# Performance work log

Measured on AMD Instinct MI355X. Metric: run time of the kernel, lower is better.

## Reference

```python
import jax, jax.numpy as jnp
import numpy as np

N = 100000   # nodes
E = 1600000  # edges (avg degree 16)
D = 128      # feature / hidden dim
C = 64       # classes
L = 4        # number of GCNII layers
ALPHA = 0.1
LAMDA = 0.5


def setup_inputs() -> dict:
    key = jax.random.key(0)
    ks = jax.random.split(key, 8)
    stdv = 1.0 / np.sqrt(D)
    x = jax.random.normal(ks[0], (N, D), jnp.float32)
    edge_src = jax.random.randint(ks[1], (E,), 0, N)
    edge_dst = jax.random.randint(ks[2], (E,), 0, N)
    edge_weight = jax.random.uniform(ks[3], (E,), jnp.float32)
    w_in = jax.random.uniform(ks[4], (D, D), jnp.float32, -stdv, stdv)
    b_in = jnp.zeros((D,), jnp.float32)
    gcn_w = jax.random.uniform(ks[5], (L, D, D), jnp.float32, -stdv, stdv)
    w_out = jax.random.uniform(ks[6], (D, C), jnp.float32, -stdv, stdv)
    b_out = jnp.zeros((C,), jnp.float32)
    return {"x": x, "edge_src": edge_src, "edge_dst": edge_dst,
            "edge_weight": edge_weight, "w_in": w_in, "b_in": b_in,
            "gcn_w": gcn_w, "w_out": w_out, "b_out": b_out}


def _spmm(edge_src, edge_dst, edge_weight, h):
    # torch.sparse.mm(adj, h): out[i] = sum_j adj[i,j] * h[j]
    # row = dst, col = src in COO terms.
    return jax.ops.segment_sum(edge_weight[:, None] * h[edge_src],
                               edge_dst, num_segments=N)


def reference(x, edge_src, edge_dst, edge_weight, w_in, b_in, gcn_w, w_out, b_out):
    h0 = jax.nn.relu(x @ w_in + b_in)          # [N, D] initial residual
    h = h0
    for l in range(L):
        # GCNConvII called with l_arg = l+1 -> theta = log(lamda/(l_arg+1) + 1)
        theta = float(np.log(LAMDA / (l + 2) + 1.0))
        hi = _spmm(edge_src, edge_dst, edge_weight, h)      # sparse SpMM
        support = (1.0 - ALPHA) * hi + ALPHA * h0           # initial-residual mix
        out = theta * (support @ gcn_w[l]) + (1.0 - theta) * support
        out = out + h                                       # identity residual
        h = jax.nn.relu(out)
    logits = h @ w_out + b_out                              # [N, C]
    return jax.nn.log_softmax(logits, axis=1)
```

## Files before the change

### kernel.cpp

```cpp
#include <hip/hip_runtime.h>
#include <hip/hip_fp16.h>
#include <math.h>

#define N_NODES 100000
#define N_EDGES 1600000
#define DIM     128
#define NCLS    64
#define ALPHA   0.1f

#define SCAN_B  98
#define NB      391
#define NF      ((size_t)N_NODES * DIM)
#define STRIPES (N_NODES / 16)
#define CHUNK   4096

typedef __attribute__((ext_vector_type(8))) _Float16 f16x8;
typedef __attribute__((ext_vector_type(4))) float    f32x4;

__device__ __forceinline__ __half2 u2h2(unsigned int u) {
    union { unsigned int u; __half2 h; } x; x.u = u; return x.h;
}
__device__ __forceinline__ unsigned int h22u(__half2 h) {
    union { unsigned int u; __half2 h; } x; x.h = h; return x.u;
}


__global__ __launch_bounds__(256) void k_hist(const int* __restrict__ dst,
                                              int* __restrict__ bucket_cnt) {
    __shared__ int hist[NB];
    int t = threadIdx.x;
    for (int b = t; b < NB; b += 256) hist[b] = 0;
    __syncthreads();
    int base = blockIdx.x * CHUNK;
    int end = min(base + CHUNK, N_EDGES);
    for (int i = base + t; i < end; i += 256)
        atomicAdd(&hist[dst[i] >> 8], 1);
    __syncthreads();
    for (int b = t; b < NB; b += 256)
        if (hist[b]) atomicAdd(&bucket_cnt[b], hist[b]);
}

__global__ __launch_bounds__(512) void k_scanb(const int* __restrict__ bucket_cnt,
                                               int* __restrict__ bucket_base,
                                               int* __restrict__ bucket_cursor) {
    __shared__ int s[512];
    int t = threadIdx.x;
    int v = (t < NB) ? bucket_cnt[t] : 0;
    s[t] = v;
    __syncthreads();
    for (int off = 1; off < 512; off <<= 1) {
        int u = (t >= off) ? s[t - off] : 0;
        __syncthreads();
        s[t] += u;
        __syncthreads();
    }
    if (t < NB) {
        int base = s[t] - v;
        bucket_base[t] = base;
        bucket_cursor[t] = base;
    }
    if (t == 0) bucket_base[NB] = N_EDGES;
}

__global__ __launch_bounds__(256) void k_part(const int* __restrict__ src,
                                              const int* __restrict__ dst,
                                              const float* __restrict__ ew,
                                              int* __restrict__ bucket_cursor,
                                              int2* __restrict__ ebuf) {
    __shared__ int lhist[NB], gbase[NB];
    int t = threadIdx.x;
    for (int b = t; b < NB; b += 256) lhist[b] = 0;
    __syncthreads();
    int base = blockIdx.x * CHUNK;
    int end = min(base + CHUNK, N_EDGES);
    for (int i = base + t; i < end; i += 256)
        atomicAdd(&lhist[dst[i] >> 8], 1);
    __syncthreads();
    for (int b = t; b < NB; b += 256) {
        int c = lhist[b];
        gbase[b] = c ? atomicAdd(&bucket_cursor[b], c) : 0;
        lhist[b] = 0;
    }
    __syncthreads();
    for (int i = base + t; i < end; i += 256) {
        int d = dst[i];
        int b = d >> 8;
        int r = atomicAdd(&lhist[b], 1);
        ebuf[gbase[b] + r] = make_int2(src[i] | ((d & 255) << 17),
                                       __float_as_int((1.0f - ALPHA) * ew[i]));
    }
}

__global__ __launch_bounds__(256) void k_deg(const int2* __restrict__ ebuf,
                                             const int* __restrict__ bucket_base,
                                             int* __restrict__ deg) {
    __shared__ int cnt[256];
    int t = threadIdx.x, b = blockIdx.x;
    cnt[t] = 0;
    __syncthreads();
    int beg = bucket_base[b], end = bucket_base[b + 1];
    for (int i = beg + t; i < end; i += 256)
        atomicAdd(&cnt[ebuf[i].x >> 17], 1);
    __syncthreads();
    int node = b * 256 + t;
    if (node < N_NODES) deg[node] = cnt[t];
}

__global__ __launch_bounds__(1024) void k_scan1(const int* __restrict__ deg,
                                                int* __restrict__ row_ptr,
                                                int* __restrict__ blocksum) {
    __shared__ int s[1024];
    int t = threadIdx.x;
    int i = blockIdx.x * 1024 + t;
    int v = (i < N_NODES) ? deg[i] : 0;
    s[t] = v;
    __syncthreads();
    for (int off = 1; off < 1024; off <<= 1) {
        int u = (t >= off) ? s[t - off] : 0;
        __syncthreads();
        s[t] += u;
        __syncthreads();
    }
    if (i < N_NODES) row_ptr[i] = s[t] - v;
    if (t == 1023) blocksum[blockIdx.x] = s[1023];
}

__global__ __launch_bounds__(128) void k_scan2(int* __restrict__ blocksum) {
    __shared__ int s[128];
    int t = threadIdx.x;
    int v = (t < SCAN_B) ? blocksum[t] : 0;
    s[t] = v;
    __syncthreads();
    for (int off = 1; off < 128; off <<= 1) {
        int u = (t >= off) ? s[t - off] : 0;
        __syncthreads();
        s[t] += u;
        __syncthreads();
    }
    if (t < SCAN_B) blocksum[t] = s[t] - v;
}

__global__ __launch_bounds__(1024) void k_scan3(int* __restrict__ row_ptr,
                                                const int* __restrict__ blocksum) {
    int t = threadIdx.x;
    int i = blockIdx.x * 1024 + t;
    if (i < N_NODES) row_ptr[i] += blocksum[blockIdx.x];
    if (i == 0) row_ptr[N_NODES] = N_EDGES;
}

__global__ __launch_bounds__(256) void k_scatter2(const int2* __restrict__ ebuf,
                                                  const int* __restrict__ bucket_base,
                                                  const int* __restrict__ row_ptr,
                                                  int2* __restrict__ colw) {
    __shared__ int lcur[256];
    int t = threadIdx.x, b = blockIdx.x;
    int node = b * 256 + t;
    lcur[t] = (node < N_NODES) ? row_ptr[node] : 0;
    __syncthreads();
    int beg = bucket_base[b], end = bucket_base[b + 1];
    for (int i = beg + t; i < end; i += 256) {
        int2 e = ebuf[i];
        int pos = atomicAdd(&lcur[e.x >> 17], 1);
        unsigned int w2 = h22u(__float2half2_rn(__int_as_float(e.y)));
        colw[pos] = make_int2(e.x & 0x1FFFF, (int)w2);
    }
}

__global__ void k_prepw(const float* __restrict__ gcnw, const float* __restrict__ wout,
                        const float* __restrict__ win, unsigned short* __restrict__ wp) {
    int tid = blockIdx.x * 256 + threadIdx.x;
    if (tid < 65536) {
        int l = tid >> 14;
        int r = tid & 16383;
        int j = r & 7, lane = (r >> 3) & 63, ch = (r >> 9) & 3, nt = r >> 11;
        int n = nt * 16 + (lane & 15);
        int k = ch * 32 + (lane >> 4) * 8 + j;
        wp[tid] = __half_as_ushort(__float2half(gcnw[l * 16384 + k * 128 + n]));
    } else if (tid < 73728) {
        int r = tid - 65536;
        int j = r & 7, lane = (r >> 3) & 63, ch = (r >> 9) & 3, nt = r >> 11;
        int n = nt * 16 + (lane & 15);
        int k = ch * 32 + (lane >> 4) * 8 + j;
        wp[tid] = __half_as_ushort(__float2half(wout[k * 64 + n]));
    } else if (tid < 90112) {
        int r = tid - 73728;
        int j = r & 7, lane = (r >> 3) & 63, ch = (r >> 9) & 3, nt = r >> 11;
        int n = nt * 16 + (lane & 15);
        int k = ch * 32 + (lane >> 4) * 8 + j;
        wp[tid] = __half_as_ushort(__float2half(win[k * 128 + n]));
    }
}

__global__ __launch_bounds__(256, 8) void k_spmm_csr(
    const int* __restrict__ row_ptr, const int2* __restrict__ colw,
    const unsigned short* __restrict__ h, const unsigned short* __restrict__ h0,
    unsigned short* __restrict__ out) {
    int node = blockIdx.x * 4 + (threadIdx.x >> 6);
    if (node >= N_NODES) return;
    int lane = threadIdx.x & 63;
    int slot = lane >> 4;
    int seg  = lane & 15;
    int beg = row_ptr[node], end = row_ptr[node + 1];

    __half2 z2 = __float2half2_rn(0.f);
    __half2 acc2[4] = {z2, z2, z2, z2};
    if (slot == 0) {
        uint4 z = *(const uint4*)(h0 + (size_t)node * DIM + seg * 8);
        __half2 al2 = __float2half2_rn(ALPHA);
        acc2[0] = __hmul2(al2, u2h2(z.x));
        acc2[1] = __hmul2(al2, u2h2(z.y));
        acc2[2] = __hmul2(al2, u2h2(z.z));
        acc2[3] = __hmul2(al2, u2h2(z.w));
    }

    int last = end - 1;
    for (int e = beg; e < end; e += 16) {
        int e0 = e + slot, e1 = e0 + 4, e2 = e0 + 8, e3 = e0 + 12;
        int2 c0 = colw[min(e0, last)];
        int2 c1 = colw[min(e1, last)];
        int2 c2 = colw[min(e2, last)];
        int2 c3 = colw[min(e3, last)];
        uint4 r0 = *(const uint4*)(h + (size_t)c0.x * DIM + seg * 8);
        uint4 r1 = *(const uint4*)(h + (size_t)c1.x * DIM + seg * 8);
        uint4 r2 = *(const uint4*)(h + (size_t)c2.x * DIM + seg * 8);
        uint4 r3 = *(const uint4*)(h + (size_t)c3.x * DIM + seg * 8);
        __half2 w0 = (e0 < end) ? u2h2((unsigned int)c0.y) : z2;
        __half2 w1 = (e1 < end) ? u2h2((unsigned int)c1.y) : z2;
        __half2 w2 = (e2 < end) ? u2h2((unsigned int)c2.y) : z2;
        __half2 w3 = (e3 < end) ? u2h2((unsigned int)c3.y) : z2;
        acc2[0] = __hfma2(w0, u2h2(r0.x), acc2[0]);
        acc2[1] = __hfma2(w0, u2h2(r0.y), acc2[1]);
        acc2[2] = __hfma2(w0, u2h2(r0.z), acc2[2]);
        acc2[3] = __hfma2(w0, u2h2(r0.w), acc2[3]);
        acc2[0] = __hfma2(w1, u2h2(r1.x), acc2[0]);
        acc2[1] = __hfma2(w1, u2h2(r1.y), acc2[1]);
        acc2[2] = __hfma2(w1, u2h2(r1.z), acc2[2]);
        acc2[3] = __hfma2(w1, u2h2(r1.w), acc2[3]);
        acc2[0] = __hfma2(w2, u2h2(r2.x), acc2[0]);
        acc2[1] = __hfma2(w2, u2h2(r2.y), acc2[1]);
        acc2[2] = __hfma2(w2, u2h2(r2.z), acc2[2]);
        acc2[3] = __hfma2(w2, u2h2(r2.w), acc2[3]);
        acc2[0] = __hfma2(w3, u2h2(r3.x), acc2[0]);
        acc2[1] = __hfma2(w3, u2h2(r3.y), acc2[1]);
        acc2[2] = __hfma2(w3, u2h2(r3.z), acc2[2]);
        acc2[3] = __hfma2(w3, u2h2(r3.w), acc2[3]);
    }

    #pragma unroll
    for (int j = 0; j < 4; j++) {
        unsigned int u = __shfl_xor(h22u(acc2[j]), 16);
        acc2[j] = __hadd2(acc2[j], u2h2(u));
        u = __shfl_xor(h22u(acc2[j]), 32);
        acc2[j] = __hadd2(acc2[j], u2h2(u));
    }

    if (slot == 0) {
        *(uint4*)(out + (size_t)node * DIM + seg * 8) =
            make_uint4(h22u(acc2[0]), h22u(acc2[1]), h22u(acc2[2]), h22u(acc2[3]));
    }
}

__global__ __launch_bounds__(256) void k_in_mfma(
    const float* __restrict__ x, const unsigned short* __restrict__ wp,
    const float* __restrict__ b_in, unsigned short* __restrict__ h0) {
    int wave = threadIdx.x >> 6, lane = threadIdx.x & 63;
    int stripe = blockIdx.x * 4 + wave;
    if (stripe >= STRIPES) return;
    int r0 = stripe * 16;
    int m = lane & 15, q = lane >> 4;

    f32x4 acc[8];
    #pragma unroll
    for (int nt = 0; nt < 8; nt++) acc[nt] = (f32x4){0.f, 0.f, 0.f, 0.f};

    const float* xr = x + (size_t)(r0 + m) * DIM + q * 8;
    #pragma unroll
    for (int ch = 0; ch < 4; ch++) {
        float4 a0 = *(const float4*)(xr + ch * 32);
        float4 a1 = *(const float4*)(xr + ch * 32 + 4);
        f16x8 a;
        a[0] = (_Float16)a0.x; a[1] = (_Float16)a0.y;
        a[2] = (_Float16)a0.z; a[3] = (_Float16)a0.w;
        a[4] = (_Float16)a1.x; a[5] = (_Float16)a1.y;
        a[6] = (_Float16)a1.z; a[7] = (_Float16)a1.w;
        #pragma unroll
        for (int nt = 0; nt < 8; nt++) {
            f16x8 b = *(const f16x8*)(wp + (((nt * 4 + ch) * 64 + lane) << 3));
            acc[nt] = __builtin_amdgcn_mfma_f32_16x16x32_f16(a, b, acc[nt], 0, 0, 0);
        }
    }

    #pragma unroll
    for (int nt = 0; nt < 8; nt++) {
        int col = nt * 16 + m;
        float bias = b_in[col];
        #pragma unroll
        for (int r = 0; r < 4; r++) {
            int row = r0 + q * 4 + r;
            h0[(size_t)row * DIM + col] =
                __half_as_ushort(__float2half(fmaxf(acc[nt][r] + bias, 0.f)));
        }
    }
}

__global__ __launch_bounds__(256) void k_layer_mfma(
    const unsigned short* __restrict__ s_in, const unsigned short* __restrict__ hprev,
    const unsigned short* __restrict__ wp, unsigned short* __restrict__ hout,
    float theta) {
    int wave = threadIdx.x >> 6, lane = threadIdx.x & 63;
    int stripe = blockIdx.x * 4 + wave;
    if (stripe >= STRIPES) return;
    int r0 = stripe * 16;
    int m = lane & 15, q = lane >> 4;
    float omt = 1.f - theta;

    f32x4 acc[8];
    #pragma unroll
    for (int nt = 0; nt < 8; nt++) acc[nt] = (f32x4){0.f, 0.f, 0.f, 0.f};

    const unsigned short* arow = s_in + (size_t)(r0 + m) * DIM + q * 8;
    #pragma unroll
    for (int ch = 0; ch < 4; ch++) {
        f16x8 a = *(const f16x8*)(arow + ch * 32);
        #pragma unroll
        for (int nt = 0; nt < 8; nt++) {
            f16x8 b = *(const f16x8*)(wp + (((nt * 4 + ch) * 64 + lane) << 3));
            acc[nt] = __builtin_amdgcn_mfma_f32_16x16x32_f16(a, b, acc[nt], 0, 0, 0);
        }
    }

    #pragma unroll
    for (int nt = 0; nt < 8; nt++) {
        int col = nt * 16 + m;
        #pragma unroll
        for (int r = 0; r < 4; r++) {
            int row = r0 + q * 4 + r;
            size_t idx = (size_t)row * DIM + col;
            float sup = __half2float(__ushort_as_half(s_in[idx]));
            float hp  = __half2float(__ushort_as_half(hprev[idx]));
            float o = theta * acc[nt][r] + omt * sup + hp;
            hout[idx] = __half_as_ushort(__float2half(fmaxf(o, 0.f)));
        }
    }
}

__global__ __launch_bounds__(256) void k_out_mfma(
    const unsigned short* __restrict__ h, const unsigned short* __restrict__ wp,
    const float* __restrict__ bo, float* __restrict__ out) {
    int wave = threadIdx.x >> 6, lane = threadIdx.x & 63;
    int stripe = blockIdx.x * 4 + wave;
    if (stripe >= STRIPES) return;
    int r0 = stripe * 16;
    int m = lane & 15, q = lane >> 4;

    f32x4 acc[4];
    #pragma unroll
    for (int nt = 0; nt < 4; nt++) acc[nt] = (f32x4){0.f, 0.f, 0.f, 0.f};

    const unsigned short* arow = h + (size_t)(r0 + m) * DIM + q * 8;
    #pragma unroll
    for (int ch = 0; ch < 4; ch++) {
        f16x8 a = *(const f16x8*)(arow + ch * 32);
        #pragma unroll
        for (int nt = 0; nt < 4; nt++) {
            f16x8 b = *(const f16x8*)(wp + (((nt * 4 + ch) * 64 + lane) << 3));
            acc[nt] = __builtin_amdgcn_mfma_f32_16x16x32_f16(a, b, acc[nt], 0, 0, 0);
        }
    }

    float v[4][4];
    #pragma unroll
    for (int nt = 0; nt < 4; nt++) {
        float bias = bo[nt * 16 + m];
        #pragma unroll
        for (int r = 0; r < 4; r++) v[nt][r] = acc[nt][r] + bias;
    }
    #pragma unroll
    for (int r = 0; r < 4; r++) {
        float mx = fmaxf(fmaxf(v[0][r], v[1][r]), fmaxf(v[2][r], v[3][r]));
        #pragma unroll
        for (int off = 1; off < 16; off <<= 1) mx = fmaxf(mx, __shfl_xor(mx, off));
        float s = 0.f;
        #pragma unroll
        for (int nt = 0; nt < 4; nt++) s += __expf(v[nt][r] - mx);
        #pragma unroll
        for (int off = 1; off < 16; off <<= 1) s += __shfl_xor(s, off);
        float lse = mx + logf(s);
        int row = r0 + q * 4 + r;
        #pragma unroll
        for (int nt = 0; nt < 4; nt++)
            out[(size_t)row * NCLS + nt * 16 + m] = v[nt][r] - lse;
    }
}

extern "C" void kernel_launch(void* const* d_in, const int* in_sizes, int n_in,
                              void* d_out, int out_size, void* d_ws, size_t ws_size,
                              hipStream_t stream) {
    const float* x    = (const float*)d_in[0];
    const int*   esrc = (const int*)d_in[1];
    const int*   edst = (const int*)d_in[2];
    const float* ew   = (const float*)d_in[3];
    const float* w_in = (const float*)d_in[4];
    const float* b_in = (const float*)d_in[5];
    const float* gcnw = (const float*)d_in[6];
    const float* wout = (const float*)d_in[7];
    const float* bout = (const float*)d_in[8];
    float* out = (float*)d_out;

    unsigned short* h0 = (unsigned short*)d_ws;
    unsigned short* hA = h0 + NF;
    unsigned short* hB = hA + NF;
    unsigned short* hi = hB + NF;
    unsigned short* wp = hi + NF;
    int2* colw = (int2*)(wp + 90112);
    int2* ebuf = colw + N_EDGES;
    int*  row_ptr       = (int*)(ebuf + N_EDGES);
    int*  deg           = row_ptr + (N_NODES + 1);
    int*  blocksum      = deg + N_NODES;
    int*  bucket_cnt    = blocksum + SCAN_B;
    int*  bucket_base   = bucket_cnt + NB;
    int*  bucket_cursor = bucket_base + (NB + 1);

    const int PART_B = (N_EDGES + CHUNK - 1) / CHUNK;
    const int MFMA_BLOCKS = (STRIPES + 3) / 4;

    k_prepw<<<(90112 + 255) / 256, 256, 0, stream>>>(gcnw, wout, w_in, wp);

    hipMemsetAsync(bucket_cnt, 0, NB * sizeof(int), stream);
    k_hist<<<PART_B, 256, 0, stream>>>(edst, bucket_cnt);
    k_scanb<<<1, 512, 0, stream>>>(bucket_cnt, bucket_base, bucket_cursor);
    k_part<<<PART_B, 256, 0, stream>>>(esrc, edst, ew, bucket_cursor, ebuf);
    k_deg<<<NB, 256, 0, stream>>>(ebuf, bucket_base, deg);
    k_scan1<<<SCAN_B, 1024, 0, stream>>>(deg, row_ptr, blocksum);
    k_scan2<<<1, 128, 0, stream>>>(blocksum);
    k_scan3<<<SCAN_B, 1024, 0, stream>>>(row_ptr, blocksum);
    k_scatter2<<<NB, 256, 0, stream>>>(ebuf, bucket_base, row_ptr, colw);

    k_in_mfma<<<MFMA_BLOCKS, 256, 0, stream>>>(x, wp + 73728, b_in, h0);

    const unsigned short* hprev = h0;
    unsigned short* bufs[2] = {hA, hB};
    for (int l = 0; l < 4; l++) {
        float theta = logf(0.5f / (float)(l + 2) + 1.0f);
        k_spmm_csr<<<(N_NODES + 3) / 4, 256, 0, stream>>>(row_ptr, colw, hprev, h0, hi);
        unsigned short* hnew = bufs[l & 1];
        k_layer_mfma<<<MFMA_BLOCKS, 256, 0, stream>>>(hi, hprev, wp + (size_t)l * 16384,
                                                      hnew, theta);
        hprev = hnew;
    }

    k_out_mfma<<<MFMA_BLOCKS, 256, 0, stream>>>(hprev, wp + 65536, bout, out);
}
```

Before: 551.7 us.

## Fuse degree count, global scan and scatter into one per-bucket sort kernel

Replaces the degree-count kernel, the three-kernel global prefix scan over node degrees, and the scatter kernel with a single per-bucket kernel. Each bucket's block counts degrees in shared memory, does a local exclusive scan, and offsets it by the bucket's base, which already serves as the global offset. It then scatters edges into CSR order. This removes four kernel launches and the global deg/blocksum round trips, at the cost of reading the bucket's edges twice within one block.

```diff
diff --git a/kernel.cpp b/kernel.cpp
--- a/kernel.cpp
+++ b/kernel.cpp
@@ -8,7 +8,6 @@
 #define NCLS    64
 #define ALPHA   0.1f
 
-#define SCAN_B  98
 #define NB      391
 #define NF      ((size_t)N_NODES * DIM)
 #define STRIPES (N_NODES / 16)
@@ -91,10 +90,10 @@
     }
 }
 
-__global__ __launch_bounds__(256) void k_deg(const int2* __restrict__ ebuf,
-                                             const int* __restrict__ bucket_base,
-                                             int* __restrict__ deg) {
-    __shared__ int cnt[256];
+__global__ __launch_bounds__(256) void k_sortbucket(
+    const int2* __restrict__ ebuf, const int* __restrict__ bucket_base,
+    int* __restrict__ row_ptr, int2* __restrict__ colw) {
+    __shared__ int cnt[256], pref[256], lcur[256];
     int t = threadIdx.x, b = blockIdx.x;
     cnt[t] = 0;
     __syncthreads();
@@ -102,62 +101,21 @@
     for (int i = beg + t; i < end; i += 256)
         atomicAdd(&cnt[ebuf[i].x >> 17], 1);
     __syncthreads();
+    int v = cnt[t];
+    pref[t] = v;
+    __syncthreads();
+    for (int off = 1; off < 256; off <<= 1) {
+        int u = (t >= off) ? pref[t - off] : 0;
+        __syncthreads();
+        pref[t] += u;
+        __syncthreads();
+    }
+    int excl = pref[t] - v;
     int node = b * 256 + t;
-    if (node < N_NODES) deg[node] = cnt[t];
-}
-
-__global__ __launch_bounds__(1024) void k_scan1(const int* __restrict__ deg,
-                                                int* __restrict__ row_ptr,
-                                                int* __restrict__ blocksum) {
-    __shared__ int s[1024];
-    int t = threadIdx.x;
-    int i = blockIdx.x * 1024 + t;
-    int v = (i < N_NODES) ? deg[i] : 0;
-    s[t] = v;
-    __syncthreads();
-    for (int off = 1; off < 1024; off <<= 1) {
-        int u = (t >= off) ? s[t - off] : 0;
-        __syncthreads();
-        s[t] += u;
-        __syncthreads();
-    }
-    if (i < N_NODES) row_ptr[i] = s[t] - v;
-    if (t == 1023) blocksum[blockIdx.x] = s[1023];
-}
-
-__global__ __launch_bounds__(128) void k_scan2(int* __restrict__ blocksum) {
-    __shared__ int s[128];
-    int t = threadIdx.x;
-    int v = (t < SCAN_B) ? blocksum[t] : 0;
-    s[t] = v;
-    __syncthreads();
-    for (int off = 1; off < 128; off <<= 1) {
-        int u = (t >= off) ? s[t - off] : 0;
-        __syncthreads();
-        s[t] += u;
-        __syncthreads();
-    }
-    if (t < SCAN_B) blocksum[t] = s[t] - v;
-}
-
-__global__ __launch_bounds__(1024) void k_scan3(int* __restrict__ row_ptr,
-                                                const int* __restrict__ blocksum) {
-    int t = threadIdx.x;
-    int i = blockIdx.x * 1024 + t;
-    if (i < N_NODES) row_ptr[i] += blocksum[blockIdx.x];
-    if (i == 0) row_ptr[N_NODES] = N_EDGES;
-}
-
-__global__ __launch_bounds__(256) void k_scatter2(const int2* __restrict__ ebuf,
-                                                  const int* __restrict__ bucket_base,
-                                                  const int* __restrict__ row_ptr,
-                                                  int2* __restrict__ colw) {
-    __shared__ int lcur[256];
-    int t = threadIdx.x, b = blockIdx.x;
-    int node = b * 256 + t;
-    lcur[t] = (node < N_NODES) ? row_ptr[node] : 0;
-    __syncthreads();
-    int beg = bucket_base[b], end = bucket_base[b + 1];
+    if (node < N_NODES) row_ptr[node] = beg + excl;
+    if (b == 0 && t == 0) row_ptr[N_NODES] = N_EDGES;
+    lcur[t] = beg + excl;
+    __syncthreads();
     for (int i = beg + t; i < end; i += 256) {
         int2 e = ebuf[i];
         int pos = atomicAdd(&lcur[e.x >> 17], 1);
@@ -415,9 +373,7 @@
     int2* colw = (int2*)(wp + 90112);
     int2* ebuf = colw + N_EDGES;
     int*  row_ptr       = (int*)(ebuf + N_EDGES);
-    int*  deg           = row_ptr + (N_NODES + 1);
-    int*  blocksum      = deg + N_NODES;
-    int*  bucket_cnt    = blocksum + SCAN_B;
+    int*  bucket_cnt    = row_ptr + (N_NODES + 1);
     int*  bucket_base   = bucket_cnt + NB;
     int*  bucket_cursor = bucket_base + (NB + 1);
 
@@ -430,11 +386,7 @@
     k_hist<<<PART_B, 256, 0, stream>>>(edst, bucket_cnt);
     k_scanb<<<1, 512, 0, stream>>>(bucket_cnt, bucket_base, bucket_cursor);
     k_part<<<PART_B, 256, 0, stream>>>(esrc, edst, ew, bucket_cursor, ebuf);
-    k_deg<<<NB, 256, 0, stream>>>(ebuf, bucket_base, deg);
-    k_scan1<<<SCAN_B, 1024, 0, stream>>>(deg, row_ptr, blocksum);
-    k_scan2<<<1, 128, 0, stream>>>(blocksum);
-    k_scan3<<<SCAN_B, 1024, 0, stream>>>(row_ptr, blocksum);
-    k_scatter2<<<NB, 256, 0, stream>>>(ebuf, bucket_base, row_ptr, colw);
+    k_sortbucket<<<NB, 256, 0, stream>>>(ebuf, bucket_base, row_ptr, colw);
 
     k_in_mfma<<<MFMA_BLOCKS, 256, 0, stream>>>(x, wp + 73728, b_in, h0);
 
```

Measured after the change: 544.8 us. No clear change (-1.3%).
